# Performance work log

Measured on AMD Instinct MI355X. Metric: run time of the kernel, lower is better.

## Reference

```python
import jax, jax.numpy as jnp
import numpy as np

N_EMBD = 768
N_HEAD = 12


def setup_inputs() -> dict:
    key = jax.random.key(0)
    k1, k2, k3, k4, k5 = jax.random.split(key, 5)
    B, T, C = 2, 2048, N_EMBD
    s = 1.0 / np.sqrt(C)
    x = jax.random.normal(k1, (B, T, C), dtype=jnp.float32)
    W_attn = jax.random.uniform(k2, (C, 3 * C), dtype=jnp.float32, minval=-s, maxval=s)
    b_attn = jax.random.uniform(k3, (3 * C,), dtype=jnp.float32, minval=-s, maxval=s)
    W_proj = jax.random.uniform(k4, (C, C), dtype=jnp.float32, minval=-s, maxval=s)
    b_proj = jax.random.uniform(k5, (C,), dtype=jnp.float32, minval=-s, maxval=s)
    return {"x": x, "W_attn": W_attn, "b_attn": b_attn, "W_proj": W_proj, "b_proj": b_proj}


def reference(x, W_attn, b_attn, W_proj, b_proj):
    B, T, C = x.shape
    H = N_HEAD
    D = C // H
    qkv = x @ W_attn + b_attn                      # [B,T,3C]
    q, k, v = jnp.split(qkv, 3, axis=-1)
    q = q.reshape(B, T, H, D).transpose(0, 2, 1, 3)  # [B,H,T,D]
    k = k.reshape(B, T, H, D).transpose(0, 2, 1, 3)
    v = v.reshape(B, T, H, D).transpose(0, 2, 1, 3)
    scale = 1.0 / jnp.sqrt(jnp.asarray(D, dtype=x.dtype))
    scores = jnp.einsum("bhqd,bhkd->bhqk", q, k) * scale  # [B,H,T,T]
    causal = jnp.tril(jnp.ones((T, T), dtype=bool))
    scores = jnp.where(causal, scores, jnp.finfo(x.dtype).min)
    attn = jax.nn.softmax(scores, axis=-1)
    y = jnp.einsum("bhqk,bhkd->bhqd", attn, v)     # [B,H,T,D]
    y = y.transpose(0, 2, 1, 3).reshape(B, T, C)
    return y @ W_proj + b_proj
```

## Files before the change

kernel.cpp:

```cpp
#include <hip/hip_runtime.h>
#include <math.h>

#define N_EMBD 768
#define N_HEAD 12
#define HEAD_DIM 64
#define SEQ 2048
#define BATCH 2

typedef __attribute__((ext_vector_type(8))) short v8s;
typedef __attribute__((ext_vector_type(4))) float v4f;

__device__ __forceinline__ unsigned short f2bf(float f) {
    union { float f; unsigned int u; } x; x.f = f;
    unsigned int u = x.u + 0x7fffu + ((x.u >> 16) & 1u);
    return (unsigned short)(u >> 16);
}
__device__ __forceinline__ float bf2f(unsigned short s) {
    union { unsigned int u; float f; } x; x.u = ((unsigned int)s) << 16;
    return x.f;
}
__device__ __forceinline__ unsigned int pack_bf16(float lo, float hi) {
    unsigned int ul = __float_as_uint(lo) + 0x8000u;
    unsigned int uh = __float_as_uint(hi) + 0x8000u;
    return __builtin_amdgcn_perm(uh, ul, 0x07060302);
}

__device__ __forceinline__ void gload_lds16(const unsigned short* g, unsigned short* l) {
    __builtin_amdgcn_global_load_lds(
        (const __attribute__((address_space(1))) void*)g,
        (__attribute__((address_space(3))) void*)l, 16, 0, 0);
}

#define QSCALE 0.1803368801111396f

__global__ __launch_bounds__(256) void prep_kernel(
    const float* __restrict__ x,
    const float* __restrict__ W_attn,
    const float* __restrict__ W_proj,
    unsigned short* __restrict__ xb,
    unsigned short* __restrict__ wta,
    unsigned short* __restrict__ wtp)
{
    __shared__ float t[32][33];
    const int blk = (int)blockIdx.x;
    if (blk < 1536) {
        const int i = (blk * 256 + threadIdx.x) * 8;
        const float4 a = *(const float4*)(x + i);
        const float4 b = *(const float4*)(x + i + 4);
        ushort4 s0, s1;
        s0.x = f2bf(a.x); s0.y = f2bf(a.y); s0.z = f2bf(a.z); s0.w = f2bf(a.w);
        s1.x = f2bf(b.x); s1.y = f2bf(b.y); s1.z = f2bf(b.z); s1.w = f2bf(b.w);
        *(ushort4*)(xb + i) = s0;
        *(ushort4*)(xb + i + 4) = s1;
        return;
    }
    const float* in; unsigned short* out; int R, C, bx, by;
    if (blk < 1536 + 1728) {
        const int b2 = blk - 1536;
        in = W_attn; out = wta; R = 768; C = 2304;
        bx = (b2 % 72) * 32; by = (b2 / 72) * 32;
    } else {
        const int b2 = blk - 3264;
        in = W_proj; out = wtp; R = 768; C = 768;
        bx = (b2 % 24) * 32; by = (b2 / 24) * 32;
    }
    const int tx = threadIdx.x & 31, ty = threadIdx.x >> 5;
#pragma unroll
    for (int i = 0; i < 32; i += 8)
        t[ty + i][tx] = in[(size_t)(by + ty + i) * C + bx + tx];
    __syncthreads();
#pragma unroll
    for (int i = 0; i < 32; i += 8)
        out[(size_t)(bx + ty + i) * R + by + tx] = f2bf(t[tx][ty + i]);
}

__global__ __launch_bounds__(256) void qkv_gemm_mfma(
    const unsigned short* __restrict__ A,
    const unsigned short* __restrict__ Bt,
    const float* __restrict__ bias,
    unsigned short* __restrict__ qg,
    unsigned short* __restrict__ kg,
    unsigned short* __restrict__ vg)
{
    __shared__ unsigned short as[2][128 * 32];
    __shared__ unsigned short bs[2][128 * 32];
    const int K = 768;
    const int tid = threadIdx.x;
    const int lane = tid & 63;
    const int w = tid >> 6;
    const int wm = w >> 1, wn = w & 1;
    const int quad = lane >> 4, c = lane & 15;
    const int bm = blockIdx.y * 128;
    const int bn = blockIdx.x * 128;

    const int srow = tid >> 2;
    const int soff = (tid & 3) * 8;
    const unsigned short* ap = A  + (size_t)(bm + srow) * K + soff;
    const unsigned short* bp = Bt + (size_t)(bn + srow) * K + soff;
    const unsigned short* ap2 = A  + (size_t)(bm + 64 + srow) * K + soff;
    const unsigned short* bp2 = Bt + (size_t)(bn + 64 + srow) * K + soff;

    v4f acc[4][4];
#pragma unroll
    for (int i = 0; i < 4; i++)
#pragma unroll
        for (int j = 0; j < 4; j++) acc[i][j] = (v4f){0.f, 0.f, 0.f, 0.f};

    gload_lds16(ap, &as[0][tid * 8]);
    gload_lds16(ap2, &as[0][(256 + tid) * 8]);
    gload_lds16(bp, &bs[0][tid * 8]);
    gload_lds16(bp2, &bs[0][(256 + tid) * 8]);

    int bufi = 0;
    for (int k0 = 0; k0 < K; k0 += 32, bufi ^= 1) {
        __syncthreads();
        if (k0 + 32 < K) {
            const int kn = k0 + 32;
            gload_lds16(ap + kn, &as[bufi ^ 1][tid * 8]);
            gload_lds16(ap2 + kn, &as[bufi ^ 1][(256 + tid) * 8]);
            gload_lds16(bp + kn, &bs[bufi ^ 1][tid * 8]);
            gload_lds16(bp2 + kn, &bs[bufi ^ 1][(256 + tid) * 8]);
        }

        v8s af[4], bf[4];
#pragma unroll
        for (int fm = 0; fm < 4; fm++)
            af[fm] = *(const v8s*)&as[bufi][(wm * 64 + fm * 16 + c) * 32 + quad * 8];
#pragma unroll
        for (int fn = 0; fn < 4; fn++)
            bf[fn] = *(const v8s*)&bs[bufi][(wn * 64 + fn * 16 + c) * 32 + quad * 8];
#pragma unroll
        for (int fm = 0; fm < 4; fm++)
#pragma unroll
            for (int fn = 0; fn < 4; fn++)
                acc[fm][fn] = __builtin_amdgcn_mfma_f32_16x16x32_bf16(af[fm], bf[fn], acc[fm][fn], 0, 0, 0);
    }

    const int which = bn / N_EMBD;
    const int rem_base = bn - which * N_EMBD;
#pragma unroll
    for (int fm = 0; fm < 4; fm++) {
        const int m0 = bm + wm * 64 + fm * 16 + quad * 4;
        const int b = m0 >> 11;
        const int t0 = m0 & (SEQ - 1);
#pragma unroll
        for (int fn = 0; fn < 4; fn++) {
            const int rem = rem_base + wn * 64 + fn * 16 + c;
            const int h = rem >> 6, d = rem & 63;
            const float bv = bias[bn + wn * 64 + fn * 16 + c];
            const size_t bh = (size_t)(b * N_HEAD + h);
            if (which == 2) {
                ushort4 o;
                o.x = f2bf(acc[fm][fn][0] + bv);
                o.y = f2bf(acc[fm][fn][1] + bv);
                o.z = f2bf(acc[fm][fn][2] + bv);
                o.w = f2bf(acc[fm][fn][3] + bv);
                *(ushort4*)(vg + (bh * 64 + d) * SEQ + t0) = o;
            } else {
                unsigned short* dst = (which == 0) ? qg : kg;
                const float sc = (which == 0) ? QSCALE : 1.0f;
#pragma unroll
                for (int r = 0; r < 4; r++)
                    dst[(bh * SEQ + t0 + r) * 64 + d] = f2bf((acc[fm][fn][r] + bv) * sc);
            }
        }
    }
}

__global__ __launch_bounds__(256) void attn_kernel(
    const unsigned short* __restrict__ qg,
    const unsigned short* __restrict__ kg,
    const unsigned short* __restrict__ vg,
    unsigned short* __restrict__ pO,
    float* __restrict__ pl)
{
    __shared__ __align__(16) unsigned short ks[2][64 * 64];
    __shared__ __align__(16) unsigned short vs[2][64 * 64];
    __shared__ __align__(16) unsigned short ps[4][16 * 64];

    const int tid  = threadIdx.x;
    const int w    = tid >> 6;
    const int lane = tid & 63;
    const int quad = lane >> 4;
    const int c    = lane & 15;

    const int bid = (int)blockIdx.x;
    const int bh  = bid % 24;
    const int c2  = 79 - (bid / 24);
    int qt, kc;
    if (c2 < 8)       { qt = c2;                    kc = 0; }
    else if (c2 < 24) { qt = 8 + ((c2 - 8) >> 1);   kc = (c2 - 8) & 1; }
    else if (c2 < 48) { qt = 16 + (c2 - 24) / 3;    kc = (c2 - 24) % 3; }
    else              { qt = 24 + ((c2 - 48) >> 2); kc = (c2 - 48) & 3; }
    const int qbase = qt * 64;

    const unsigned short* qrow = qg + (size_t)bh * SEQ * 64;
    const unsigned short* krow = kg + (size_t)bh * SEQ * 64;
    const unsigned short* vrow = vg + (size_t)bh * 64 * SEQ;

    const unsigned short* qp = qrow + (size_t)(qbase + w * 16 + c) * 64 + quad * 8;
    const v8s bq0 = *(const v8s*)(qp);
    const v8s bq1 = *(const v8s*)(qp + 32);

    const int r0 = tid >> 3;
    const int ch0 = (tid & 7) ^ (r0 & 7);
    const unsigned short* kp0 = krow + (size_t)r0 * 64 + ch0 * 8;
    const unsigned short* vp0 = vrow + (size_t)r0 * SEQ + ch0 * 8;

    const int swz0 = ((quad ^ (c & 7)) * 8);
    const int swz1 = swz0 ^ 32;

    v4f oacc[4];
#pragma unroll
    for (int d = 0; d < 4; d++) oacc[d] = (v4f){0.f, 0.f, 0.f, 0.f};
    float l_acc = 0.f;

    const int q_lane = qbase + w * 16 + c;
    unsigned int* pw32 = (unsigned int*)&ps[w][0];
    const int psq = c & 7;

    const int kt0 = kc * 8;
    const int kt1 = min(kt0 + 8, qt + 1);

    {
        const int key0 = kt0 * 64;
        const int b = kt0 & 1;
        gload_lds16(kp0 + (size_t)key0 * 64, &ks[b][tid * 8]);
        gload_lds16(kp0 + (size_t)(key0 + 32) * 64, &ks[b][(256 + tid) * 8]);
        gload_lds16(vp0 + key0, &vs[b][tid * 8]);
        gload_lds16(vp0 + 32 * SEQ + key0, &vs[b][(256 + tid) * 8]);
    }

    for (int kt = kt0; kt < kt1; kt++) {
        const int b = kt & 1;
        __syncthreads();
        if (kt + 1 < kt1) {
            const int key0n = (kt + 1) * 64;
            gload_lds16(kp0 + (size_t)key0n * 64, &ks[b ^ 1][tid * 8]);
            gload_lds16(kp0 + (size_t)(key0n + 32) * 64, &ks[b ^ 1][(256 + tid) * 8]);
            gload_lds16(vp0 + key0n, &vs[b ^ 1][tid * 8]);
            gload_lds16(vp0 + 32 * SEQ + key0n, &vs[b ^ 1][(256 + tid) * 8]);
        }
        const int key0 = kt * 64;

        v4f sacc[4];
#pragma unroll
        for (int n = 0; n < 4; n++) {
            const int rb = (n * 16 + c) * 64;
            const v8s ak0 = *(const v8s*)&ks[b][rb + swz0];
            const v8s ak1 = *(const v8s*)&ks[b][rb + swz1];
            v4f s = (v4f){0.f, 0.f, 0.f, 0.f};
            s = __builtin_amdgcn_mfma_f32_16x16x32_bf16(ak0, bq0, s, 0, 0, 0);
            s = __builtin_amdgcn_mfma_f32_16x16x32_bf16(ak1, bq1, s, 0, 0, 0);
            sacc[n] = s;
        }

        if (kt == qt) {
            const int kb = key0 + quad * 4;
#pragma unroll
            for (int n = 0; n < 4; n++)
#pragma unroll
                for (int r = 0; r < 4; r++)
                    if (kb + n * 16 + r > q_lane) sacc[n][r] = -1e30f;
        }

#pragma unroll
        for (int n = 0; n < 4; n++) {
            const float p0 = exp2f(sacc[n][0]);
            const float p1 = exp2f(sacc[n][1]);
            const float p2 = exp2f(sacc[n][2]);
            const float p3 = exp2f(sacc[n][3]);
            l_acc += (p0 + p1) + (p2 + p3);
            const int sswz = (2 * n + (quad >> 1)) ^ psq;
            const int dw = c * 32 + sswz * 4 + (quad & 1) * 2;
            pw32[dw]     = pack_bf16(p0, p1);
            pw32[dw + 1] = pack_bf16(p2, p3);
        }

        const v8s ap0 = *(const v8s*)&ps[w][c * 64 + swz0];
        const v8s ap1 = *(const v8s*)&ps[w][c * 64 + swz1];
#pragma unroll
        for (int d = 0; d < 4; d++) {
            const int rb = (d * 16 + c) * 64;
            const v8s bv0 = *(const v8s*)&vs[b][rb + swz0];
            const v8s bv1 = *(const v8s*)&vs[b][rb + swz1];
            oacc[d] = __builtin_amdgcn_mfma_f32_16x16x32_bf16(ap0, bv0, oacc[d], 0, 0, 0);
            oacc[d] = __builtin_amdgcn_mfma_f32_16x16x32_bf16(ap1, bv1, oacc[d], 0, 0, 0);
        }
    }

    l_acc += __shfl_xor(l_acc, 16, 64);
    l_acc += __shfl_xor(l_acc, 32, 64);

    const size_t pidx = (size_t)bh * 80 + c2;
    unsigned short* po = pO + pidx * 4096;
#pragma unroll
    for (int r = 0; r < 4; r++) {
        const int row = w * 16 + quad * 4 + r;
#pragma unroll
        for (int d = 0; d < 4; d++)
            po[row * 64 + d * 16 + c] = f2bf(oacc[d][r]);
    }
    if (lane < 16)
        pl[pidx * 64 + w * 16 + c] = l_acc;
}

__global__ __launch_bounds__(256) void combine_kernel(
    const unsigned short* __restrict__ pO,
    const float* __restrict__ pl,
    unsigned short* __restrict__ y)
{
    const int qt = (int)blockIdx.x;
    const int bh = (int)blockIdx.y;
    int base, nc;
    if (qt < 8)       { base = qt;                 nc = 1; }
    else if (qt < 16) { base = 8 + 2 * (qt - 8);   nc = 2; }
    else if (qt < 24) { base = 24 + 3 * (qt - 16); nc = 3; }
    else              { base = 48 + 4 * (qt - 24); nc = 4; }

    const int row = threadIdx.x >> 2;
    const int colg = (threadIdx.x & 3) * 16;

    float denom = 0.f;
    for (int i = 0; i < nc; i++)
        denom += pl[((size_t)bh * 80 + base + i) * 64 + row];
    const float inv = 1.0f / denom;

    float acc[16];
#pragma unroll
    for (int j = 0; j < 16; j++) acc[j] = 0.f;
    for (int i = 0; i < nc; i++) {
        const unsigned short* po = pO + ((size_t)bh * 80 + base + i) * 4096 + row * 64 + colg;
        ushort4 u0 = *(const ushort4*)(po + 0);
        ushort4 u1 = *(const ushort4*)(po + 4);
        ushort4 u2 = *(const ushort4*)(po + 8);
        ushort4 u3 = *(const ushort4*)(po + 12);
        acc[0]  += bf2f(u0.x); acc[1]  += bf2f(u0.y);
        acc[2]  += bf2f(u0.z); acc[3]  += bf2f(u0.w);
        acc[4]  += bf2f(u1.x); acc[5]  += bf2f(u1.y);
        acc[6]  += bf2f(u1.z); acc[7]  += bf2f(u1.w);
        acc[8]  += bf2f(u2.x); acc[9]  += bf2f(u2.y);
        acc[10] += bf2f(u2.z); acc[11] += bf2f(u2.w);
        acc[12] += bf2f(u3.x); acc[13] += bf2f(u3.y);
        acc[14] += bf2f(u3.z); acc[15] += bf2f(u3.w);
    }

    const int b = bh / N_HEAD;
    const int h = bh - b * N_HEAD;
    const int t = qt * 64 + row;
    unsigned short* yr = y + ((size_t)(b * SEQ + t)) * N_EMBD + h * 64 + colg;
    ushort4 o0, o1, o2, o3;
    o0.x = f2bf(acc[0] * inv);  o0.y = f2bf(acc[1] * inv);
    o0.z = f2bf(acc[2] * inv);  o0.w = f2bf(acc[3] * inv);
    o1.x = f2bf(acc[4] * inv);  o1.y = f2bf(acc[5] * inv);
    o1.z = f2bf(acc[6] * inv);  o1.w = f2bf(acc[7] * inv);
    o2.x = f2bf(acc[8] * inv);  o2.y = f2bf(acc[9] * inv);
    o2.z = f2bf(acc[10] * inv); o2.w = f2bf(acc[11] * inv);
    o3.x = f2bf(acc[12] * inv); o3.y = f2bf(acc[13] * inv);
    o3.z = f2bf(acc[14] * inv); o3.w = f2bf(acc[15] * inv);
    *(ushort4*)(yr + 0)  = o0;
    *(ushort4*)(yr + 4)  = o1;
    *(ushort4*)(yr + 8)  = o2;
    *(ushort4*)(yr + 12) = o3;
}

__global__ __launch_bounds__(256) void proj_gemm_mfma(
    const unsigned short* __restrict__ A,
    const unsigned short* __restrict__ Bt,
    const float* __restrict__ bias,
    float* __restrict__ out)
{
    __shared__ unsigned short as[2][128 * 32];
    __shared__ unsigned short bs[2][128 * 32];
    const int K = 768;
    const int tid = threadIdx.x;
    const int lane = tid & 63;
    const int w = tid >> 6;
    const int wm = w >> 1, wn = w & 1;
    const int quad = lane >> 4, c = lane & 15;
    const int bm = blockIdx.y * 128;
    const int bn = blockIdx.x * 128;

    const int srow = tid >> 2;
    const int soff = (tid & 3) * 8;
    const unsigned short* ap = A  + (size_t)(bm + srow) * K + soff;
    const unsigned short* bp = Bt + (size_t)(bn + srow) * K + soff;
    const unsigned short* ap2 = A  + (size_t)(bm + 64 + srow) * K + soff;
    const unsigned short* bp2 = Bt + (size_t)(bn + 64 + srow) * K + soff;

    v4f acc[4][4];
#pragma unroll
    for (int i = 0; i < 4; i++)
#pragma unroll
        for (int j = 0; j < 4; j++) acc[i][j] = (v4f){0.f, 0.f, 0.f, 0.f};

    gload_lds16(ap, &as[0][tid * 8]);
    gload_lds16(ap2, &as[0][(256 + tid) * 8]);
    gload_lds16(bp, &bs[0][tid * 8]);
    gload_lds16(bp2, &bs[0][(256 + tid) * 8]);

    int bufi = 0;
    for (int k0 = 0; k0 < K; k0 += 32, bufi ^= 1) {
        __syncthreads();
        if (k0 + 32 < K) {
            const int kn = k0 + 32;
            gload_lds16(ap + kn, &as[bufi ^ 1][tid * 8]);
            gload_lds16(ap2 + kn, &as[bufi ^ 1][(256 + tid) * 8]);
            gload_lds16(bp + kn, &bs[bufi ^ 1][tid * 8]);
            gload_lds16(bp2 + kn, &bs[bufi ^ 1][(256 + tid) * 8]);
        }

        v8s af[4], bf[4];
#pragma unroll
        for (int fm = 0; fm < 4; fm++)
            af[fm] = *(const v8s*)&as[bufi][(wm * 64 + fm * 16 + c) * 32 + quad * 8];
#pragma unroll
        for (int fn = 0; fn < 4; fn++)
            bf[fn] = *(const v8s*)&bs[bufi][(wn * 64 + fn * 16 + c) * 32 + quad * 8];
#pragma unroll
        for (int fm = 0; fm < 4; fm++)
#pragma unroll
            for (int fn = 0; fn < 4; fn++)
                acc[fm][fn] = __builtin_amdgcn_mfma_f32_16x16x32_bf16(af[fm], bf[fn], acc[fm][fn], 0, 0, 0);
    }

#pragma unroll
    for (int fm = 0; fm < 4; fm++) {
        const int m0 = bm + wm * 64 + fm * 16 + quad * 4;
#pragma unroll
        for (int fn = 0; fn < 4; fn++) {
            const int n = bn + wn * 64 + fn * 16 + c;
            const float bv = bias[n];
#pragma unroll
            for (int r = 0; r < 4; r++)
                out[(size_t)(m0 + r) * N_EMBD + n] = acc[fm][fn][r] + bv;
        }
    }
}

extern "C" void kernel_launch(void* const* d_in, const int* in_sizes, int n_in,
                              void* d_out, int out_size, void* d_ws, size_t ws_size,
                              hipStream_t stream) {
    const float* x      = (const float*)d_in[0];
    const float* W_attn = (const float*)d_in[1];
    const float* b_attn = (const float*)d_in[2];
    const float* W_proj = (const float*)d_in[3];
    const float* b_proj = (const float*)d_in[4];
    float* out = (float*)d_out;

    const size_t QSZ = (size_t)BATCH * N_HEAD * SEQ * HEAD_DIM;

    unsigned short* base = (unsigned short*)d_ws;
    unsigned short* xb  = base;
    unsigned short* wta = base + QSZ;
    unsigned short* pO  = base;
    float* pl = (float*)(base + (size_t)1920 * 4096);
    unsigned short* wtp = (unsigned short*)(pl + 1920 * 64);
    unsigned short* qg  = wtp + (size_t)N_EMBD * N_EMBD;
    unsigned short* kg  = qg + QSZ;
    unsigned short* vg  = kg + QSZ;
    unsigned short* yb  = vg + QSZ;

    prep_kernel<<<dim3(3840), 256, 0, stream>>>(x, W_attn, W_proj, xb, wta, wtp);
    qkv_gemm_mfma<<<dim3(18, 32), 256, 0, stream>>>(xb, wta, b_attn, qg, kg, vg);
    attn_kernel<<<dim3(80 * 24), 256, 0, stream>>>(qg, kg, vg, pO, pl);
    combine_kernel<<<dim3(32, BATCH * N_HEAD), 256, 0, stream>>>(pO, pl, yb);
    proj_gemm_mfma<<<dim3(6, 32), 256, 0, stream>>>(yb, wtp, b_proj, out);
}
```

Measured before the change: 162.1 us.

## Enlarge attention query tile to 128 rows so each K/V tile is reused twice

The attention kernel now handles 128 query rows per block instead of 64, with each wave computing two 16-row groups against every staged K/V tile. Each K/V tile loaded into LDS now feeds twice as much MFMA work, which cuts global and LDS traffic per FLOP. The split schedule, partial-output layout and combine kernel are rescaled to 40 chunks per head. The cost is more registers per thread, a larger P scratch buffer in LDS, half as many blocks (which can hurt load balance and occupancy), and more wasted masked work on diagonal tiles.

```diff
diff --git a/kernel.cpp b/kernel.cpp
--- a/kernel.cpp
+++ b/kernel.cpp
@@ -176,7 +176,7 @@
 {
     __shared__ __align__(16) unsigned short ks[2][64 * 64];
     __shared__ __align__(16) unsigned short vs[2][64 * 64];
-    __shared__ __align__(16) unsigned short ps[4][16 * 64];
+    __shared__ __align__(16) unsigned short ps[128 * 64];
 
     const int tid  = threadIdx.x;
     const int w    = tid >> 6;
@@ -186,21 +186,25 @@
 
     const int bid = (int)blockIdx.x;
     const int bh  = bid % 24;
-    const int c2  = 79 - (bid / 24);
-    int qt, kc;
-    if (c2 < 8)       { qt = c2;                    kc = 0; }
-    else if (c2 < 24) { qt = 8 + ((c2 - 8) >> 1);   kc = (c2 - 8) & 1; }
-    else if (c2 < 48) { qt = 16 + (c2 - 24) / 3;    kc = (c2 - 24) % 3; }
-    else              { qt = 24 + ((c2 - 48) >> 2); kc = (c2 - 48) & 3; }
-    const int qbase = qt * 64;
+    const int c2  = 39 - (bid / 24);
+    int qb, kc;
+    if (c2 < 4)       { qb = c2;                 kc = 0; }
+    else if (c2 < 12) { qb = 4 + ((c2 - 4) >> 1);  kc = (c2 - 4) & 1; }
+    else if (c2 < 24) { qb = 8 + (c2 - 12) / 3;    kc = (c2 - 12) % 3; }
+    else              { qb = 12 + ((c2 - 24) >> 2); kc = (c2 - 24) & 3; }
+    const int qbase = qb * 128;
 
     const unsigned short* qrow = qg + (size_t)bh * SEQ * 64;
     const unsigned short* krow = kg + (size_t)bh * SEQ * 64;
     const unsigned short* vrow = vg + (size_t)bh * 64 * SEQ;
 
-    const unsigned short* qp = qrow + (size_t)(qbase + w * 16 + c) * 64 + quad * 8;
-    const v8s bq0 = *(const v8s*)(qp);
-    const v8s bq1 = *(const v8s*)(qp + 32);
+    v8s bq[2][2];
+#pragma unroll
+    for (int g = 0; g < 2; g++) {
+        const unsigned short* qp = qrow + (size_t)(qbase + w * 32 + g * 16 + c) * 64 + quad * 8;
+        bq[g][0] = *(const v8s*)(qp);
+        bq[g][1] = *(const v8s*)(qp + 32);
+    }
 
     const int r0 = tid >> 3;
     const int ch0 = (tid & 7) ^ (r0 & 7);
@@ -210,17 +214,20 @@
     const int swz0 = ((quad ^ (c & 7)) * 8);
     const int swz1 = swz0 ^ 32;
 
-    v4f oacc[4];
-#pragma unroll
-    for (int d = 0; d < 4; d++) oacc[d] = (v4f){0.f, 0.f, 0.f, 0.f};
-    float l_acc = 0.f;
-
-    const int q_lane = qbase + w * 16 + c;
-    unsigned int* pw32 = (unsigned int*)&ps[w][0];
+    v4f oacc[2][4];
+#pragma unroll
+    for (int g = 0; g < 2; g++)
+#pragma unroll
+        for (int d = 0; d < 4; d++) oacc[g][d] = (v4f){0.f, 0.f, 0.f, 0.f};
+    float l_acc[2] = {0.f, 0.f};
+
+    unsigned int* pw32 = (unsigned int*)ps;
     const int psq = c & 7;
-
+    const int qmin_w = qbase + w * 32;
+
+    const int ktmax = 2 * qb + 2;
     const int kt0 = kc * 8;
-    const int kt1 = min(kt0 + 8, qt + 1);
+    const int kt1 = min(kt0 + 8, ktmax);
 
     {
         const int key0 = kt0 * 64;
@@ -243,66 +250,93 @@
         }
         const int key0 = kt * 64;
 
-        v4f sacc[4];
+        v4f sacc[4][2];
 #pragma unroll
         for (int n = 0; n < 4; n++) {
             const int rb = (n * 16 + c) * 64;
             const v8s ak0 = *(const v8s*)&ks[b][rb + swz0];
             const v8s ak1 = *(const v8s*)&ks[b][rb + swz1];
-            v4f s = (v4f){0.f, 0.f, 0.f, 0.f};
-            s = __builtin_amdgcn_mfma_f32_16x16x32_bf16(ak0, bq0, s, 0, 0, 0);
-            s = __builtin_amdgcn_mfma_f32_16x16x32_bf16(ak1, bq1, s, 0, 0, 0);
-            sacc[n] = s;
-        }
-
-        if (kt == qt) {
+#pragma unroll
+            for (int g = 0; g < 2; g++) {
+                v4f s = (v4f){0.f, 0.f, 0.f, 0.f};
+                s = __builtin_amdgcn_mfma_f32_16x16x32_bf16(ak0, bq[g][0], s, 0, 0, 0);
+                s = __builtin_amdgcn_mfma_f32_16x16x32_bf16(ak1, bq[g][1], s, 0, 0, 0);
+                sacc[n][g] = s;
+            }
+        }
+
+        if (key0 + 63 > qmin_w) {
             const int kb = key0 + quad * 4;
 #pragma unroll
-            for (int n = 0; n < 4; n++)
-#pragma unroll
-                for (int r = 0; r < 4; r++)
-                    if (kb + n * 16 + r > q_lane) sacc[n][r] = -1e30f;
-        }
-
-#pragma unroll
-        for (int n = 0; n < 4; n++) {
-            const float p0 = exp2f(sacc[n][0]);
-            const float p1 = exp2f(sacc[n][1]);
-            const float p2 = exp2f(sacc[n][2]);
-            const float p3 = exp2f(sacc[n][3]);
-            l_acc += (p0 + p1) + (p2 + p3);
-            const int sswz = (2 * n + (quad >> 1)) ^ psq;
-            const int dw = c * 32 + sswz * 4 + (quad & 1) * 2;
-            pw32[dw]     = pack_bf16(p0, p1);
-            pw32[dw + 1] = pack_bf16(p2, p3);
-        }
-
-        const v8s ap0 = *(const v8s*)&ps[w][c * 64 + swz0];
-        const v8s ap1 = *(const v8s*)&ps[w][c * 64 + swz1];
+            for (int g = 0; g < 2; g++) {
+                const int q_lane = qmin_w + g * 16 + c;
+#pragma unroll
+                for (int n = 0; n < 4; n++)
+#pragma unroll
+                    for (int r = 0; r < 4; r++)
+                        if (kb + n * 16 + r > q_lane) sacc[n][g][r] = -1e30f;
+            }
+        }
+
+#pragma unroll
+        for (int g = 0; g < 2; g++) {
+            unsigned int* pbase = pw32 + (w * 32 + g * 16 + c) * 32;
+#pragma unroll
+            for (int n = 0; n < 4; n++) {
+                const float p0 = exp2f(sacc[n][g][0]);
+                const float p1 = exp2f(sacc[n][g][1]);
+                const float p2 = exp2f(sacc[n][g][2]);
+                const float p3 = exp2f(sacc[n][g][3]);
+                l_acc[g] += (p0 + p1) + (p2 + p3);
+                const int sswz = (2 * n + (quad >> 1)) ^ psq;
+                const int dw = sswz * 4 + (quad & 1) * 2;
+                pbase[dw]     = pack_bf16(p0, p1);
+                pbase[dw + 1] = pack_bf16(p2, p3);
+            }
+        }
+
+        v8s ap[2][2];
+#pragma unroll
+        for (int g = 0; g < 2; g++) {
+            const int prow = (w * 32 + g * 16 + c) * 64;
+            ap[g][0] = *(const v8s*)&ps[prow + swz0];
+            ap[g][1] = *(const v8s*)&ps[prow + swz1];
+        }
 #pragma unroll
         for (int d = 0; d < 4; d++) {
             const int rb = (d * 16 + c) * 64;
             const v8s bv0 = *(const v8s*)&vs[b][rb + swz0];
             const v8s bv1 = *(const v8s*)&vs[b][rb + swz1];
-            oacc[d] = __builtin_amdgcn_mfma_f32_16x16x32_bf16(ap0, bv0, oacc[d], 0, 0, 0);
-            oacc[d] = __builtin_amdgcn_mfma_f32_16x16x32_bf16(ap1, bv1, oacc[d], 0, 0, 0);
-        }
-    }
-
-    l_acc += __shfl_xor(l_acc, 16, 64);
-    l_acc += __shfl_xor(l_acc, 32, 64);
-
-    const size_t pidx = (size_t)bh * 80 + c2;
-    unsigned short* po = pO + pidx * 4096;
-#pragma unroll
-    for (int r = 0; r < 4; r++) {
-        const int row = w * 16 + quad * 4 + r;
-#pragma unroll
-        for (int d = 0; d < 4; d++)
-            po[row * 64 + d * 16 + c] = f2bf(oacc[d][r]);
-    }
-    if (lane < 16)
-        pl[pidx * 64 + w * 16 + c] = l_acc;
+#pragma unroll
+            for (int g = 0; g < 2; g++) {
+                oacc[g][d] = __builtin_amdgcn_mfma_f32_16x16x32_bf16(ap[g][0], bv0, oacc[g][d], 0, 0, 0);
+                oacc[g][d] = __builtin_amdgcn_mfma_f32_16x16x32_bf16(ap[g][1], bv1, oacc[g][d], 0, 0, 0);
+            }
+        }
+    }
+
+#pragma unroll
+    for (int g = 0; g < 2; g++) {
+        l_acc[g] += __shfl_xor(l_acc[g], 16, 64);
+        l_acc[g] += __shfl_xor(l_acc[g], 32, 64);
+    }
+
+    const size_t pidx = (size_t)bh * 40 + c2;
+    unsigned short* po = pO + pidx * 8192;
+#pragma unroll
+    for (int g = 0; g < 2; g++) {
+#pragma unroll
+        for (int r = 0; r < 4; r++) {
+            const int row = w * 32 + g * 16 + quad * 4 + r;
+#pragma unroll
+            for (int d = 0; d < 4; d++)
+                po[row * 64 + d * 16 + c] = f2bf(oacc[g][d][r]);
+        }
+    }
+    if (lane < 16) {
+        pl[pidx * 128 + w * 32 + c]      = l_acc[0];
+        pl[pidx * 128 + w * 32 + 16 + c] = l_acc[1];
+    }
 }
 
 __global__ __launch_bounds__(256) void combine_kernel(
@@ -310,58 +344,51 @@
     const float* __restrict__ pl,
     unsigned short* __restrict__ y)
 {
-    const int qt = (int)blockIdx.x;
+    const int qb = (int)blockIdx.x;
     const int bh = (int)blockIdx.y;
     int base, nc;
-    if (qt < 8)       { base = qt;                 nc = 1; }
-    else if (qt < 16) { base = 8 + 2 * (qt - 8);   nc = 2; }
-    else if (qt < 24) { base = 24 + 3 * (qt - 16); nc = 3; }
-    else              { base = 48 + 4 * (qt - 24); nc = 4; }
-
-    const int row = threadIdx.x >> 2;
-    const int colg = (threadIdx.x & 3) * 16;
+    if (qb < 4)       { base = qb;                 nc = 1; }
+    else if (qb < 8)  { base = 4 + 2 * (qb - 4);   nc = 2; }
+    else if (qb < 12) { base = 12 + 3 * (qb - 8);  nc = 3; }
+    else              { base = 24 + 4 * (qb - 12); nc = 4; }
+
+    const int row = threadIdx.x >> 1;
+    const int colg = (threadIdx.x & 1) * 32;
 
     float denom = 0.f;
     for (int i = 0; i < nc; i++)
-        denom += pl[((size_t)bh * 80 + base + i) * 64 + row];
+        denom += pl[((size_t)bh * 40 + base + i) * 128 + row];
     const float inv = 1.0f / denom;
 
-    float acc[16];
-#pragma unroll
-    for (int j = 0; j < 16; j++) acc[j] = 0.f;
+    float acc[32];
+#pragma unroll
+    for (int j = 0; j < 32; j++) acc[j] = 0.f;
     for (int i = 0; i < nc; i++) {
-        const unsigned short* po = pO + ((size_t)bh * 80 + base + i) * 4096 + row * 64 + colg;
-        ushort4 u0 = *(const ushort4*)(po + 0);
-        ushort4 u1 = *(const ushort4*)(po + 4);
-        ushort4 u2 = *(const ushort4*)(po + 8);
-        ushort4 u3 = *(const ushort4*)(po + 12);
-        acc[0]  += bf2f(u0.x); acc[1]  += bf2f(u0.y);
-        acc[2]  += bf2f(u0.z); acc[3]  += bf2f(u0.w);
-        acc[4]  += bf2f(u1.x); acc[5]  += bf2f(u1.y);
-        acc[6]  += bf2f(u1.z); acc[7]  += bf2f(u1.w);
-        acc[8]  += bf2f(u2.x); acc[9]  += bf2f(u2.y);
-        acc[10] += bf2f(u2.z); acc[11] += bf2f(u2.w);
-        acc[12] += bf2f(u3.x); acc[13] += bf2f(u3.y);
-        acc[14] += bf2f(u3.z); acc[15] += bf2f(u3.w);
+        const unsigned short* po = pO + ((size_t)bh * 40 + base + i) * 8192 + row * 64 + colg;
+#pragma unroll
+        for (int j8 = 0; j8 < 4; j8++) {
+            ushort4 u0 = *(const ushort4*)(po + j8 * 8);
+            ushort4 u1 = *(const ushort4*)(po + j8 * 8 + 4);
+            acc[j8 * 8 + 0] += bf2f(u0.x); acc[j8 * 8 + 1] += bf2f(u0.y);
+            acc[j8 * 8 + 2] += bf2f(u0.z); acc[j8 * 8 + 3] += bf2f(u0.w);
+            acc[j8 * 8 + 4] += bf2f(u1.x); acc[j8 * 8 + 5] += bf2f(u1.y);
+            acc[j8 * 8 + 6] += bf2f(u1.z); acc[j8 * 8 + 7] += bf2f(u1.w);
+        }
     }
 
     const int b = bh / N_HEAD;
     const int h = bh - b * N_HEAD;
-    const int t = qt * 64 + row;
+    const int t = qb * 128 + row;
     unsigned short* yr = y + ((size_t)(b * SEQ + t)) * N_EMBD + h * 64 + colg;
-    ushort4 o0, o1, o2, o3;
-    o0.x = f2bf(acc[0] * inv);  o0.y = f2bf(acc[1] * inv);
-    o0.z = f2bf(acc[2] * inv);  o0.w = f2bf(acc[3] * inv);
-    o1.x = f2bf(acc[4] * inv);  o1.y = f2bf(acc[5] * inv);
-    o1.z = f2bf(acc[6] * inv);  o1.w = f2bf(acc[7] * inv);
-    o2.x = f2bf(acc[8] * inv);  o2.y = f2bf(acc[9] * inv);
-    o2.z = f2bf(acc[10] * inv); o2.w = f2bf(acc[11] * inv);
-    o3.x = f2bf(acc[12] * inv); o3.y = f2bf(acc[13] * inv);
-    o3.z = f2bf(acc[14] * inv); o3.w = f2bf(acc[15] * inv);
-    *(ushort4*)(yr + 0)  = o0;
-    *(ushort4*)(yr + 4)  = o1;
-    *(ushort4*)(yr + 8)  = o2;
-    *(ushort4*)(yr + 12) = o3;
+#pragma unroll
+    for (int j4 = 0; j4 < 8; j4++) {
+        ushort4 o;
+        o.x = f2bf(acc[j4 * 4 + 0] * inv);
+        o.y = f2bf(acc[j4 * 4 + 1] * inv);
+        o.z = f2bf(acc[j4 * 4 + 2] * inv);
+        o.w = f2bf(acc[j4 * 4 + 3] * inv);
+        *(ushort4*)(yr + j4 * 4) = o;
+    }
 }
 
 __global__ __launch_bounds__(256) void proj_gemm_mfma(
@@ -454,8 +481,8 @@
     unsigned short* xb  = base;
     unsigned short* wta = base + QSZ;
     unsigned short* pO  = base;
-    float* pl = (float*)(base + (size_t)1920 * 4096);
-    unsigned short* wtp = (unsigned short*)(pl + 1920 * 64);
+    float* pl = (float*)(base + (size_t)960 * 8192);
+    unsigned short* wtp = (unsigned short*)(pl + 960 * 128);
     unsigned short* qg  = wtp + (size_t)N_EMBD * N_EMBD;
     unsigned short* kg  = qg + QSZ;
     unsigned short* vg  = kg + QSZ;
@@ -463,7 +490,7 @@
 
     prep_kernel<<<dim3(3840), 256, 0, stream>>>(x, W_attn, W_proj, xb, wta, wtp);
     qkv_gemm_mfma<<<dim3(18, 32), 256, 0, stream>>>(xb, wta, b_attn, qg, kg, vg);
-    attn_kernel<<<dim3(80 * 24), 256, 0, stream>>>(qg, kg, vg, pO, pl);
-    combine_kernel<<<dim3(32, BATCH * N_HEAD), 256, 0, stream>>>(pO, pl, yb);
+    attn_kernel<<<dim3(40 * 24), 256, 0, stream>>>(qg, kg, vg, pO, pl);
+    combine_kernel<<<dim3(16, BATCH * N_HEAD), 256, 0, stream>>>(pO, pl, yb);
     proj_gemm_mfma<<<dim3(6, 32), 256, 0, stream>>>(yb, wtp, b_proj, out);
 }
```

After: 168.5 us. +3.9%, slower.
